# Optimization experiments

Hardware: AMD Instinct MI355X
Metric: run time of the kernel (lower is better)

The kernel has to match this reference:

```python
import jax, jax.numpy as jnp
import numpy as np

B, S, E, H = 2, 2048, 1024, 16
D = E // H  # head_dim = 64


def setup_inputs() -> dict:
    key = jax.random.key(0)
    ks = jax.random.split(key, 5)
    return {
        "hidden_states": jax.random.normal(ks[0], (B, S, E), jnp.float32),
        "c_attn_w": jax.random.normal(ks[1], (E, 3 * E), jnp.float32) * 0.02,
        "c_attn_b": jnp.zeros((3 * E,), jnp.float32),
        "c_proj_w": jax.random.normal(ks[2], (E, E), jnp.float32) * 0.02,
        "c_proj_b": jnp.zeros((E,), jnp.float32),
    }


def reference(hidden_states, c_attn_w, c_attn_b, c_proj_w, c_proj_b):
    # Conv1D: x @ w + b -> qkv [B, S, 3E]
    qkv = hidden_states @ c_attn_w + c_attn_b
    q, k, v = jnp.split(qkv, 3, axis=-1)
    # [B, H, S, D]
    q = q.reshape(B, S, H, D).transpose(0, 2, 1, 3)
    k = k.reshape(B, S, H, D).transpose(0, 2, 1, 3)
    v = v.reshape(B, S, H, D).transpose(0, 2, 1, 3)
    # scores [B, H, S, S], scaled by sqrt(head_dim)
    scores = jnp.einsum("bhqd,bhkd->bhqk", q, k) / jnp.sqrt(jnp.asarray(D, q.dtype))
    causal = jnp.tril(jnp.ones((S, S), bool))  # [S, S]
    mask_value = jnp.finfo(scores.dtype).min
    scores = jnp.where(causal, scores, mask_value)
    attn = jax.nn.softmax(scores, axis=-1)
    # attn @ V -> [B, H, S, D] -> [B, S, E]
    out = jnp.einsum("bhqk,bhkd->bhqd", attn, v)
    out = out.transpose(0, 2, 1, 3).reshape(B, S, E)
    return out @ c_proj_w + c_proj_b
```

## Files before the change

kernel.cpp:

```cpp
#include <hip/hip_runtime.h>

using bf16 = __bf16;
typedef __bf16 bf16x8 __attribute__((ext_vector_type(8)));
typedef __bf16 bf16x4 __attribute__((ext_vector_type(4)));
typedef float  f32x4  __attribute__((ext_vector_type(4)));

#define MFMA16(a, b, c) __builtin_amdgcn_mfma_f32_16x16x32_bf16((a), (b), (c), 0, 0, 0)

static constexpr int S = 2048, E = 1024;
static constexpr float CSCALE = 0.18033688011112042f;

__device__ __forceinline__ void gld16(const bf16* g, bf16* l) {
    __builtin_amdgcn_global_load_lds((const __attribute__((address_space(1))) unsigned*)g,
                                     (__attribute__((address_space(3))) unsigned*)l, 16, 0, 0);
}

__global__ __launch_bounds__(256) void k_prep(const float* __restrict__ hs, const float* __restrict__ w0,
                                              const float* __restrict__ w1, bf16* __restrict__ A0,
                                              bf16* __restrict__ Wt0, bf16* __restrict__ Wt1) {
    __shared__ float tile[32][33];
    const int bx = blockIdx.x;
    if (bx < 4096) {
        int i = (bx * 256 + threadIdx.x) * 4;
        float4 v = *(const float4*)(hs + i);
        bf16x4 o = { (bf16)v.x, (bf16)v.y, (bf16)v.z, (bf16)v.w };
        *(bf16x4*)(A0 + i) = o;
        return;
    }
    const float* in;
    bf16* outp;
    int K, N, nb, kb;
    if (bx < 4096 + 3072) {
        int j = bx - 4096; in = w0; outp = Wt0; K = 1024; N = 3072; nb = j % 96; kb = j / 96;
    } else {
        int j = bx - 7168; in = w1; outp = Wt1; K = 1024; N = 1024; nb = j % 32; kb = j / 32;
    }
    const int bxx = nb * 32, byy = kb * 32;
    const int tx = threadIdx.x & 31, ty = threadIdx.x >> 5;
#pragma unroll
    for (int i = 0; i < 32; i += 8)
        tile[ty + i][tx] = in[(long)(byy + ty + i) * N + bxx + tx];
    __syncthreads();
#pragma unroll
    for (int i = 0; i < 32; i += 8)
        outp[(long)(bxx + ty + i) * K + byy + tx] = (bf16)tile[tx][ty + i];
}

__global__ __launch_bounds__(512, 2) void k_gemm_qkv(const bf16* __restrict__ A, const bf16* __restrict__ Bt,
                                                     const float* __restrict__ bias, bf16* __restrict__ Qs,
                                                     bf16* __restrict__ Kf, bf16* __restrict__ Vf, int Kk) {
    __shared__ __align__(16) char smem[131072];
    bf16* sA = (bf16*)smem;
    bf16* sB = (bf16*)(smem + 65536);

    const int NT = Kk >> 5;

    const int cpx = gridDim.x >> 3;
    const int bid = blockIdx.x;
    const int sid = (bid & 7) * cpx + (bid >> 3);
    const long bm = (long)(sid & 15) * 256;
    const int bnT = sid >> 4;
    const long bn = (long)bnT * 256;

    const int tid = threadIdx.x;
    const int w = tid >> 6, lane = tid & 63;
    const int col = lane & 15, quad = lane >> 4;
    const int wr = w >> 2, wc = w & 3;
    const int wrow = wr * 128, wcol = wc * 64;

    const int c0 = tid, c1 = 512 + tid;
    const int r0 = c0 >> 2, g0 = (c0 & 3) ^ ((r0 >> 1) & 3);
    const int r1 = c1 >> 2, g1 = (c1 & 3) ^ ((r1 >> 1) & 3);
    const bf16* gA0 = A + (bm + r0) * Kk + g0 * 8;
    const bf16* gA1 = A + (bm + r1) * Kk + g1 * 8;
    const bf16* gB0 = Bt + (bn + r0) * Kk + g0 * 8;
    const bf16* gB1 = Bt + (bn + r1) * Kk + g1 * 8;

    f32x4 acc[8][4] = {};

#pragma unroll
    for (int tt = 0; tt < 3; ++tt) {
        bf16* dA = sA + tt * 8192;
        bf16* dB = sB + tt * 8192;
        gld16(gA0 + tt * 32, dA + w * 512);
        gld16(gA1 + tt * 32, dA + 4096 + w * 512);
        gld16(gB0 + tt * 32, dB + w * 512);
        gld16(gB1 + tt * 32, dB + 4096 + w * 512);
    }
    asm volatile("s_waitcnt vmcnt(8)" ::: "memory");
    __builtin_amdgcn_s_barrier();

#pragma unroll 1
    for (int t = 0; t < NT; ++t) {
        const bf16* sAs = sA + (t & 3) * 8192;
        const bf16* sBs = sB + (t & 3) * 8192;
        const int ts = t + 3;
        bf16* dA = sA + (ts & 3) * 8192;
        bf16* dB = sB + (ts & 3) * 8192;

        bf16x8 bfr[4], af[4];
#pragma unroll
        for (int nt = 0; nt < 4; ++nt) {
            const int row = wcol + nt * 16 + col;
            bfr[nt] = *(const bf16x8*)(sBs + row * 32 + ((quad ^ ((row >> 1) & 3)) * 8));
        }
#pragma unroll
        for (int mt = 0; mt < 4; ++mt) {
            const int row = wrow + mt * 16 + col;
            af[mt] = *(const bf16x8*)(sAs + row * 32 + ((quad ^ ((row >> 1) & 3)) * 8));
        }
        if (ts < NT) {
            gld16(gA0 + ts * 32, dA + w * 512);
            gld16(gA1 + ts * 32, dA + 4096 + w * 512);
        }
        __builtin_amdgcn_s_barrier();
        __builtin_amdgcn_s_setprio(1);
#pragma unroll
        for (int mt = 0; mt < 4; ++mt)
#pragma unroll
            for (int nt = 0; nt < 4; ++nt)
                acc[mt][nt] = MFMA16(af[mt], bfr[nt], acc[mt][nt]);
        __builtin_amdgcn_s_setprio(0);
        __builtin_amdgcn_s_barrier();

#pragma unroll
        for (int mt = 0; mt < 4; ++mt) {
            const int row = wrow + 64 + mt * 16 + col;
            af[mt] = *(const bf16x8*)(sAs + row * 32 + ((quad ^ ((row >> 1) & 3)) * 8));
        }
        if (ts < NT) {
            gld16(gB0 + ts * 32, dB + w * 512);
            gld16(gB1 + ts * 32, dB + 4096 + w * 512);
        }
        __builtin_amdgcn_s_barrier();
        __builtin_amdgcn_s_setprio(1);
#pragma unroll
        for (int mt = 0; mt < 4; ++mt)
#pragma unroll
            for (int nt = 0; nt < 4; ++nt)
                acc[4 + mt][nt] = MFMA16(af[mt], bfr[nt], acc[4 + mt][nt]);
        __builtin_amdgcn_s_setprio(0);
        if (t < NT - 3)       asm volatile("s_waitcnt vmcnt(8)" ::: "memory");
        else if (t == NT - 3) asm volatile("s_waitcnt vmcnt(4)" ::: "memory");
        else if (t == NT - 2) asm volatile("s_waitcnt vmcnt(0)" ::: "memory");
        __builtin_amdgcn_s_barrier();
    }

    const int seg = bnT >> 2;

    if (seg == 0) {
#pragma unroll
        for (int nt = 0; nt < 4; ++nt) {
            const long gc = bn + wcol + nt * 16 + col;
            const float bv = bias[gc];
#pragma unroll
            for (int mt = 0; mt < 8; ++mt) {
                const long gr = bm + wrow + mt * 16 + quad * 4;
#pragma unroll
                for (int r = 0; r < 4; ++r)
                    Qs[(gr + r) * 1024 + gc] = (bf16)((acc[mt][nt][r] + bv) * CSCALE);
            }
        }
        return;
    }

    bf16* myT = (bf16*)smem + w * (64 * 72);
    const int bmi = (int)bm;
    const int b = bmi >> 11;
    const int ktw = ((bmi & 2047) >> 6) + wr * 2;
    float bv[4];
#pragma unroll
    for (int nt = 0; nt < 4; ++nt) bv[nt] = bias[bn + wcol + nt * 16 + col];

    if (seg == 1) {
        const int head = (((int)bn - 1024) >> 6) + wc;
        const int bh = b * 16 + head;
#pragma unroll
        for (int p = 0; p < 2; ++p) {
#pragma unroll
            for (int mt2 = 0; mt2 < 4; ++mt2)
#pragma unroll
                for (int nt = 0; nt < 4; ++nt)
#pragma unroll
                    for (int r = 0; r < 4; ++r)
                        myT[(mt2 * 16 + quad * 4 + r) * 72 + nt * 16 + col] =
                            (bf16)(acc[p * 4 + mt2][nt][r] + bv[nt]);
#pragma unroll
            for (int mtp = 0; mtp < 4; ++mtp)
#pragma unroll
                for (int half = 0; half < 2; ++half) {
                    bf16x8 ch = *(const bf16x8*)(myT + (mtp * 16 + col) * 72 + half * 32 + quad * 8);
                    const long chunk = ((long)(bh * 32 + ktw + p) * 8 + mtp * 2 + half) * 64 + lane;
                    *(bf16x8*)(Kf + chunk * 8) = ch;
                }
        }
    } else {
        const int head = (((int)bn - 2048) >> 6) + wc;
        const int bh = b * 16 + head;
#pragma unroll
        for (int p = 0; p < 2; ++p) {
#pragma unroll
            for (int nt = 0; nt < 4; ++nt)
#pragma unroll
                for (int mt2 = 0; mt2 < 4; ++mt2) {
                    bf16x4 pk = { (bf16)(acc[p * 4 + mt2][nt][0] + bv[nt]),
                                  (bf16)(acc[p * 4 + mt2][nt][1] + bv[nt]),
                                  (bf16)(acc[p * 4 + mt2][nt][2] + bv[nt]),
                                  (bf16)(acc[p * 4 + mt2][nt][3] + bv[nt]) };
                    *(bf16x4*)(myT + (nt * 16 + col) * 72 + mt2 * 16 + quad * 4) = pk;
                }
#pragma unroll
            for (int dt = 0; dt < 4; ++dt)
#pragma unroll
                for (int ks = 0; ks < 2; ++ks) {
                    bf16x8 ch = *(const bf16x8*)(myT + (dt * 16 + col) * 72 + ks * 32 + quad * 8);
                    const long chunk = ((long)(bh * 32 + ktw + p) * 8 + dt * 2 + ks) * 64 + lane;
                    *(bf16x8*)(Vf + chunk * 8) = ch;
                }
        }
    }
}

__global__ __launch_bounds__(256) void k_gemm_bt64(const bf16* __restrict__ A, const bf16* __restrict__ Bt,
                                                    const float* __restrict__ bias, float* __restrict__ Cout,
                                                    int Mm, int Nn, int Kk) {
    const int bm = blockIdx.x * 64;
    const int bn = blockIdx.y * 128;
    const int tid = threadIdx.x;
    const int w = tid >> 6, lane = tid & 63;
    const int wm = (w >> 1) * 32, wn = (w & 1) * 64;
    const int col = lane & 15, quad = lane >> 4;

    __shared__ bf16 sA[64 * 64];
    __shared__ bf16 sB[128 * 64];

    const bf16* pA[2]; bf16* lA[2];
#pragma unroll
    for (int i = 0; i < 2; i++) {
        const int c = i * 256 + w * 64 + lane;
        const int r = c >> 3, sl = (c & 7) ^ (r & 7);
        pA[i] = A + (long)(bm + r) * Kk + sl * 8;
        lA[i] = sA + i * 2048 + w * 512;
    }
    const bf16* pB[4]; bf16* lB[4];
#pragma unroll
    for (int i = 0; i < 4; i++) {
        const int c = i * 256 + w * 64 + lane;
        const int r = c >> 3, sl = (c & 7) ^ (r & 7);
        pB[i] = Bt + (long)(bn + r) * Kk + sl * 8;
        lB[i] = sB + i * 2048 + w * 512;
    }

    f32x4 acc[2][4] = {};

    for (int k0 = 0; k0 < Kk; k0 += 64) {
        __syncthreads();
#pragma unroll
        for (int i = 0; i < 2; i++) gld16(pA[i] + k0, lA[i]);
#pragma unroll
        for (int i = 0; i < 4; i++) gld16(pB[i] + k0, lB[i]);
        __syncthreads();
#pragma unroll
        for (int h = 0; h < 2; h++) {
            bf16x8 af[2], bfr[4];
#pragma unroll
            for (int mt = 0; mt < 2; mt++) {
                const int row = wm + mt * 16 + col;
                af[mt] = *(const bf16x8*)(sA + row * 64 + (((h * 4 + quad) ^ (col & 7)) * 8));
            }
#pragma unroll
            for (int nt = 0; nt < 4; nt++) {
                const int row = wn + nt * 16 + col;
                bfr[nt] = *(const bf16x8*)(sB + row * 64 + (((h * 4 + quad) ^ (col & 7)) * 8));
            }
#pragma unroll
            for (int mt = 0; mt < 2; mt++)
#pragma unroll
                for (int nt = 0; nt < 4; nt++)
                    acc[mt][nt] = MFMA16(af[mt], bfr[nt], acc[mt][nt]);
        }
    }

#pragma unroll
    for (int mt = 0; mt < 2; mt++) {
        const int gr = bm + wm + mt * 16 + quad * 4;
#pragma unroll
        for (int nt = 0; nt < 4; nt++) {
            const int gc = bn + wn + nt * 16 + col;
            const float bv = bias[gc];
#pragma unroll
            for (int r = 0; r < 4; r++)
                Cout[(long)(gr + r) * Nn + gc] = acc[mt][nt][r] + bv;
        }
    }
}

__global__ __launch_bounds__(128) void k_attn(const bf16* __restrict__ Qs, const bf16* __restrict__ Kf,
                                              const bf16* __restrict__ Vf, bf16* __restrict__ out) {
    const int bh = blockIdx.x & 31;
    const int tp = blockIdx.x >> 5;
    const int b = bh >> 4, h = bh & 15;
    const int tid = threadIdx.x;
    const int w = tid >> 6, lane = tid & 63;
    const int col = lane & 15, quad = lane >> 4;

    __shared__ bf16 sP[2][32 * 72];
    __shared__ float M[2][64][36];
    bf16* pw = sP[w];

    const bf16* kfb = Kf + ((long)bh << 17) + lane * 8;
    const bf16* vfb = Vf + ((long)bh << 17) + lane * 8;

#pragma unroll 1
    for (int sel = 0; sel < 2; sel++) {
        const int t = sel ? 63 - tp : tp;
        const int q0 = t * 32;
        const int nkt = (t >> 1) + 1;
        const int kA = nkt >> 1;
        const int kbeg = w ? kA : 0;
        const int kend = w ? nkt : kA;

        bf16x8 bq[2][2];
#pragma unroll
        for (int qg = 0; qg < 2; qg++) {
            const bf16* qp = Qs + (long)(b * S + q0 + qg * 16 + col) * E + h * 64 + quad * 8;
            bq[qg][0] = *(const bf16x8*)(qp);
            bq[qg][1] = *(const bf16x8*)(qp + 32);
        }
        float m_[2] = { -1e30f, -1e30f }, l_[2] = { 0.f, 0.f };
        f32x4 o[2][4] = {};

#pragma unroll 1
        for (int kt = kbeg; kt < kend; kt++) {
            bf16x8 kfr[4][2], vfr[4][2];
#pragma unroll
            for (int mt = 0; mt < 4; mt++)
#pragma unroll
                for (int half = 0; half < 2; half++)
                    kfr[mt][half] = *(const bf16x8*)(kfb + ((long)(kt * 8 + mt * 2 + half) << 9));
#pragma unroll
            for (int dt = 0; dt < 4; dt++)
#pragma unroll
                for (int ks = 0; ks < 2; ks++)
                    vfr[dt][ks] = *(const bf16x8*)(vfb + ((long)(kt * 8 + dt * 2 + ks) << 9));

            f32x4 s[2][4];
#pragma unroll
            for (int mt = 0; mt < 4; mt++)
#pragma unroll
                for (int qg = 0; qg < 2; qg++) {
                    f32x4 z = {};
                    z = MFMA16(kfr[mt][0], bq[qg][0], z);
                    z = MFMA16(kfr[mt][1], bq[qg][1], z);
                    s[qg][mt] = z;
                }
            if (kt == nkt - 1) {
#pragma unroll
                for (int qg = 0; qg < 2; qg++) {
                    const int qrow = q0 + qg * 16 + col;
#pragma unroll
                    for (int mt = 0; mt < 4; mt++)
#pragma unroll
                        for (int r = 0; r < 4; r++)
                            if (kt * 64 + mt * 16 + quad * 4 + r > qrow) s[qg][mt][r] = -1e30f;
                }
            }
#pragma unroll
            for (int qg = 0; qg < 2; qg++) {
                float cm = -1e30f;
#pragma unroll
                for (int mt = 0; mt < 4; mt++)
#pragma unroll
                    for (int r = 0; r < 4; r++) cm = fmaxf(cm, s[qg][mt][r]);
                cm = fmaxf(cm, __shfl_xor(cm, 16));
                cm = fmaxf(cm, __shfl_xor(cm, 32));
                const float mnew = fmaxf(m_[qg], cm);
                const float alpha = __builtin_amdgcn_exp2f(m_[qg] - mnew);
                m_[qg] = mnew;
                float rs = 0.f;
#pragma unroll
                for (int mt = 0; mt < 4; mt++)
#pragma unroll
                    for (int r = 0; r < 4; r++) {
                        float pe = __builtin_amdgcn_exp2f(s[qg][mt][r] - mnew);
                        s[qg][mt][r] = pe;
                        rs += pe;
                    }
                l_[qg] = l_[qg] * alpha + rs;
#pragma unroll
                for (int dt = 0; dt < 4; dt++)
#pragma unroll
                    for (int r = 0; r < 4; r++) o[qg][dt][r] *= alpha;
#pragma unroll
                for (int mt = 0; mt < 4; mt++) {
                    bf16x4 pk = { (bf16)s[qg][mt][0], (bf16)s[qg][mt][1],
                                  (bf16)s[qg][mt][2], (bf16)s[qg][mt][3] };
                    *(bf16x4*)(pw + (qg * 16 + col) * 72 + mt * 16 + quad * 4) = pk;
                }
            }
#pragma unroll
            for (int ks = 0; ks < 2; ks++) {
                bf16x8 ap[2];
#pragma unroll
                for (int qg = 0; qg < 2; qg++)
                    ap[qg] = *(const bf16x8*)(pw + (qg * 16 + col) * 72 + ks * 32 + quad * 8);
#pragma unroll
                for (int dt = 0; dt < 4; dt++)
#pragma unroll
                    for (int qg = 0; qg < 2; qg++)
                        o[qg][dt] = MFMA16(vfr[dt][ks], ap[qg], o[qg][dt]);
            }
        }

#pragma unroll
        for (int qg = 0; qg < 2; qg++) {
            float lt = l_[qg];
            lt += __shfl_xor(lt, 16);
            lt += __shfl_xor(lt, 32);
            l_[qg] = lt;
        }

        if (w == 0) {
#pragma unroll
            for (int qg = 0; qg < 2; qg++) {
#pragma unroll
                for (int dt = 0; dt < 4; dt++)
                    *(f32x4*)&M[sel][lane][qg * 16 + dt * 4] = o[qg][dt];
                M[sel][lane][32 + qg * 2] = m_[qg];
                M[sel][lane][33 + qg * 2] = l_[qg];
            }
        }
        __syncthreads();
        if (w == 1) {
#pragma unroll
            for (int qg = 0; qg < 2; qg++) {
                const float m0 = M[sel][lane][32 + qg * 2];
                const float l0 = M[sel][lane][33 + qg * 2];
                const float mm = fmaxf(m0, m_[qg]);
                const float a0 = __builtin_amdgcn_exp2f(m0 - mm);
                const float a1 = __builtin_amdgcn_exp2f(m_[qg] - mm);
                const float li = 1.f / (l0 * a0 + l_[qg] * a1);
                bf16* op = out + (long)(b * S + q0 + qg * 16 + col) * E + h * 64 + quad * 4;
#pragma unroll
                for (int dt = 0; dt < 4; dt++) {
                    f32x4 o0 = *(const f32x4*)&M[sel][lane][qg * 16 + dt * 4];
                    bf16x4 ov;
#pragma unroll
                    for (int r = 0; r < 4; r++)
                        ov[r] = (bf16)((o0[r] * a0 + o[qg][dt][r] * a1) * li);
                    *(bf16x4*)(op + dt * 16) = ov;
                }
            }
        }
    }
}

extern "C" void kernel_launch(void* const* d_in, const int* in_sizes, int n_in,
                              void* d_out, int out_size, void* d_ws, size_t ws_size,
                              hipStream_t stream) {
    const float* hs = (const float*)d_in[0];
    const float* w0 = (const float*)d_in[1];
    const float* b0 = (const float*)d_in[2];
    const float* w1 = (const float*)d_in[3];
    const float* b1 = (const float*)d_in[4];
    float* outp = (float*)d_out;

    char* ws = (char*)d_ws;
    bf16* A0    = (bf16*)(ws);
    bf16* Wt0   = (bf16*)(ws + 8388608);
    bf16* Wt1   = (bf16*)(ws + 14680064);
    bf16* Qs    = (bf16*)(ws + 16777216);
    bf16* Kf    = (bf16*)(ws + 25165824);
    bf16* Vf    = (bf16*)(ws + 33554432);
    bf16* attnO = (bf16*)(ws + 41943040);

    k_prep<<<8192, 256, 0, stream>>>(hs, w0, w1, A0, Wt0, Wt1);
    k_gemm_qkv<<<192, 512, 0, stream>>>(A0, Wt0, b0, Qs, Kf, Vf, 1024);
    k_attn<<<1024, 128, 0, stream>>>(Qs, Kf, Vf, attnO);
    k_gemm_bt64<<<dim3(64, 8), 256, 0, stream>>>(attnO, Wt1, b1, outp, 4096, 1024, 1024);
}
```

Before: 172.8 us.

## Retile QKV GEMM to 128x192 blocks with 6 waves and triple buffering

The QKV projection GEMM moves from 256x256 tiles with 8 waves and a 4-stage buffer to 128x192 tiles with 6 waves and a 3-stage LDS ring. The grid grows from 192 to 512 blocks, which fills the 256 CUs better and lets about 3 blocks sit on each CU thanks to the smaller LDS footprint. Load assignment is redistributed across waves, and the epilogue is simplified to one 64-row pass per wave. The trade-off is less operand reuse per tile and more global and LDS traffic per FLOP.

```diff
diff --git a/kernel.cpp b/kernel.cpp
--- a/kernel.cpp
+++ b/kernel.cpp
@@ -46,73 +46,76 @@
         outp[(long)(bxx + ty + i) * K + byy + tx] = (bf16)tile[tx][ty + i];
 }
 
-__global__ __launch_bounds__(512, 2) void k_gemm_qkv(const bf16* __restrict__ A, const bf16* __restrict__ Bt,
+__global__ __launch_bounds__(384, 3) void k_gemm_qkv(const bf16* __restrict__ A, const bf16* __restrict__ Bt,
                                                      const float* __restrict__ bias, bf16* __restrict__ Qs,
                                                      bf16* __restrict__ Kf, bf16* __restrict__ Vf, int Kk) {
-    __shared__ __align__(16) char smem[131072];
+    __shared__ __align__(16) char smem[61440];
     bf16* sA = (bf16*)smem;
-    bf16* sB = (bf16*)(smem + 65536);
+    bf16* sB = (bf16*)(smem + 24576);
 
     const int NT = Kk >> 5;
 
-    const int cpx = gridDim.x >> 3;
     const int bid = blockIdx.x;
-    const int sid = (bid & 7) * cpx + (bid >> 3);
-    const long bm = (long)(sid & 15) * 256;
-    const int bnT = sid >> 4;
-    const long bn = (long)bnT * 256;
+    const int sid = (bid & 7) * 64 + (bid >> 3);
+    const long bm = (long)(sid & 31) * 128;
+    const long bn = (long)(sid >> 5) * 192;
 
     const int tid = threadIdx.x;
     const int w = tid >> 6, lane = tid & 63;
     const int col = lane & 15, quad = lane >> 4;
-    const int wr = w >> 2, wc = w & 3;
-    const int wrow = wr * 128, wcol = wc * 64;
-
-    const int c0 = tid, c1 = 512 + tid;
-    const int r0 = c0 >> 2, g0 = (c0 & 3) ^ ((r0 >> 1) & 3);
-    const int r1 = c1 >> 2, g1 = (c1 & 3) ^ ((r1 >> 1) & 3);
-    const bf16* gA0 = A + (bm + r0) * Kk + g0 * 8;
-    const bf16* gA1 = A + (bm + r1) * Kk + g1 * 8;
-    const bf16* gB0 = Bt + (bn + r0) * Kk + g0 * 8;
-    const bf16* gB1 = Bt + (bn + r1) * Kk + g1 * 8;
-
-    f32x4 acc[8][4] = {};
-
-#pragma unroll
-    for (int tt = 0; tt < 3; ++tt) {
-        bf16* dA = sA + tt * 8192;
-        bf16* dB = sB + tt * 8192;
-        gld16(gA0 + tt * 32, dA + w * 512);
-        gld16(gA1 + tt * 32, dA + 4096 + w * 512);
-        gld16(gB0 + tt * 32, dB + w * 512);
-        gld16(gB1 + tt * 32, dB + 4096 + w * 512);
-    }
-    asm volatile("s_waitcnt vmcnt(8)" ::: "memory");
+    const int wc = w % 3, wr = w / 3;
+    const int wrow = wr * 64, wcol = wc * 64;
+
+    const int nch = (w < 2) ? 4 : 3;
+    const bf16* gsrc[4];
+    bf16* ldst[4];
+    int sstep[4];
+#pragma unroll
+    for (int j = 0; j < 4; ++j) {
+        const int c = w + 6 * j;
+        const bool a = (c < 8);
+        const int cl = a ? c : (c - 8);
+        const int r = cl * 16 + (lane >> 2);
+        const int kc = (lane & 3) ^ ((r >> 1) & 3);
+        gsrc[j] = (a ? A + (bm + r) * Kk : Bt + (bn + r) * Kk) + kc * 8;
+        ldst[j] = (a ? sA : sB) + r * 32 + (lane & 3) * 8;
+        sstep[j] = a ? 4096 : 6144;
+    }
+
+    f32x4 acc[4][4] = {};
+
+#pragma unroll
+    for (int tt = 0; tt < 2; ++tt)
+#pragma unroll
+        for (int j = 0; j < 4; ++j)
+            if (j < nch) gld16(gsrc[j] + tt * 32, ldst[j] + tt * sstep[j]);
+    if (w < 2) asm volatile("s_waitcnt vmcnt(4)" ::: "memory");
+    else       asm volatile("s_waitcnt vmcnt(3)" ::: "memory");
     __builtin_amdgcn_s_barrier();
 
+    int slot = 0, wslot = 2;
 #pragma unroll 1
     for (int t = 0; t < NT; ++t) {
-        const bf16* sAs = sA + (t & 3) * 8192;
-        const bf16* sBs = sB + (t & 3) * 8192;
-        const int ts = t + 3;
-        bf16* dA = sA + (ts & 3) * 8192;
-        bf16* dB = sB + (ts & 3) * 8192;
-
-        bf16x8 bfr[4], af[4];
+        const bf16* sAs = sA + slot * 4096;
+        const bf16* sBs = sB + slot * 6144;
+
+        if (t + 2 < NT) {
+#pragma unroll
+            for (int j = 0; j < 4; ++j)
+                if (j < nch) gld16(gsrc[j] + (t + 2) * 32, ldst[j] + wslot * sstep[j]);
+        }
+
+        bf16x8 af[4], bfr[4];
+#pragma unroll
+        for (int mt = 0; mt < 4; ++mt) {
+            const int row = wrow + mt * 16 + col;
+            af[mt] = *(const bf16x8*)(sAs + row * 32 + ((quad ^ ((row >> 1) & 3)) * 8));
+        }
 #pragma unroll
         for (int nt = 0; nt < 4; ++nt) {
             const int row = wcol + nt * 16 + col;
             bfr[nt] = *(const bf16x8*)(sBs + row * 32 + ((quad ^ ((row >> 1) & 3)) * 8));
         }
-#pragma unroll
-        for (int mt = 0; mt < 4; ++mt) {
-            const int row = wrow + mt * 16 + col;
-            af[mt] = *(const bf16x8*)(sAs + row * 32 + ((quad ^ ((row >> 1) & 3)) * 8));
-        }
-        if (ts < NT) {
-            gld16(gA0 + ts * 32, dA + w * 512);
-            gld16(gA1 + ts * 32, dA + 4096 + w * 512);
-        }
         __builtin_amdgcn_s_barrier();
         __builtin_amdgcn_s_setprio(1);
 #pragma unroll
@@ -121,103 +124,79 @@
             for (int nt = 0; nt < 4; ++nt)
                 acc[mt][nt] = MFMA16(af[mt], bfr[nt], acc[mt][nt]);
         __builtin_amdgcn_s_setprio(0);
+        if (t < NT - 2) {
+            if (w < 2) asm volatile("s_waitcnt vmcnt(4)" ::: "memory");
+            else       asm volatile("s_waitcnt vmcnt(3)" ::: "memory");
+        } else {
+            asm volatile("s_waitcnt vmcnt(0)" ::: "memory");
+        }
         __builtin_amdgcn_s_barrier();
 
-#pragma unroll
-        for (int mt = 0; mt < 4; ++mt) {
-            const int row = wrow + 64 + mt * 16 + col;
-            af[mt] = *(const bf16x8*)(sAs + row * 32 + ((quad ^ ((row >> 1) & 3)) * 8));
-        }
-        if (ts < NT) {
-            gld16(gB0 + ts * 32, dB + w * 512);
-            gld16(gB1 + ts * 32, dB + 4096 + w * 512);
-        }
-        __builtin_amdgcn_s_barrier();
-        __builtin_amdgcn_s_setprio(1);
-#pragma unroll
-        for (int mt = 0; mt < 4; ++mt)
-#pragma unroll
-            for (int nt = 0; nt < 4; ++nt)
-                acc[4 + mt][nt] = MFMA16(af[mt], bfr[nt], acc[4 + mt][nt]);
-        __builtin_amdgcn_s_setprio(0);
-        if (t < NT - 3)       asm volatile("s_waitcnt vmcnt(8)" ::: "memory");
-        else if (t == NT - 3) asm volatile("s_waitcnt vmcnt(4)" ::: "memory");
-        else if (t == NT - 2) asm volatile("s_waitcnt vmcnt(0)" ::: "memory");
-        __builtin_amdgcn_s_barrier();
-    }
-
-    const int seg = bnT >> 2;
+        slot = (slot == 2) ? 0 : slot + 1;
+        wslot = (wslot == 2) ? 0 : wslot + 1;
+    }
+
+    const long gc0 = bn + wcol;
+    const int seg = (int)(gc0 >> 10);
+    float bv[4];
+#pragma unroll
+    for (int nt = 0; nt < 4; ++nt) bv[nt] = bias[gc0 + nt * 16 + col];
 
     if (seg == 0) {
 #pragma unroll
         for (int nt = 0; nt < 4; ++nt) {
-            const long gc = bn + wcol + nt * 16 + col;
-            const float bv = bias[gc];
-#pragma unroll
-            for (int mt = 0; mt < 8; ++mt) {
+            const long gc = gc0 + nt * 16 + col;
+#pragma unroll
+            for (int mt = 0; mt < 4; ++mt) {
                 const long gr = bm + wrow + mt * 16 + quad * 4;
 #pragma unroll
                 for (int r = 0; r < 4; ++r)
-                    Qs[(gr + r) * 1024 + gc] = (bf16)((acc[mt][nt][r] + bv) * CSCALE);
+                    Qs[(gr + r) * 1024 + gc] = (bf16)((acc[mt][nt][r] + bv[nt]) * CSCALE);
             }
         }
         return;
     }
 
-    bf16* myT = (bf16*)smem + w * (64 * 72);
+    bf16* myT = (bf16*)smem + w * 4608;
     const int bmi = (int)bm;
     const int b = bmi >> 11;
-    const int ktw = ((bmi & 2047) >> 6) + wr * 2;
-    float bv[4];
-#pragma unroll
-    for (int nt = 0; nt < 4; ++nt) bv[nt] = bias[bn + wcol + nt * 16 + col];
+    const int ktw = ((bmi & 2047) >> 6) + wr;
+    const int head = (int)((gc0 & 1023) >> 6);
+    const int bh = b * 16 + head;
 
     if (seg == 1) {
-        const int head = (((int)bn - 1024) >> 6) + wc;
-        const int bh = b * 16 + head;
-#pragma unroll
-        for (int p = 0; p < 2; ++p) {
-#pragma unroll
-            for (int mt2 = 0; mt2 < 4; ++mt2)
-#pragma unroll
-                for (int nt = 0; nt < 4; ++nt)
-#pragma unroll
-                    for (int r = 0; r < 4; ++r)
-                        myT[(mt2 * 16 + quad * 4 + r) * 72 + nt * 16 + col] =
-                            (bf16)(acc[p * 4 + mt2][nt][r] + bv[nt]);
-#pragma unroll
-            for (int mtp = 0; mtp < 4; ++mtp)
-#pragma unroll
-                for (int half = 0; half < 2; ++half) {
-                    bf16x8 ch = *(const bf16x8*)(myT + (mtp * 16 + col) * 72 + half * 32 + quad * 8);
-                    const long chunk = ((long)(bh * 32 + ktw + p) * 8 + mtp * 2 + half) * 64 + lane;
-                    *(bf16x8*)(Kf + chunk * 8) = ch;
-                }
-        }
+#pragma unroll
+        for (int mt = 0; mt < 4; ++mt)
+#pragma unroll
+            for (int nt = 0; nt < 4; ++nt)
+#pragma unroll
+                for (int r = 0; r < 4; ++r)
+                    myT[(mt * 16 + quad * 4 + r) * 72 + nt * 16 + col] = (bf16)(acc[mt][nt][r] + bv[nt]);
+#pragma unroll
+        for (int mtp = 0; mtp < 4; ++mtp)
+#pragma unroll
+            for (int half = 0; half < 2; ++half) {
+                bf16x8 ch = *(const bf16x8*)(myT + (mtp * 16 + col) * 72 + half * 32 + quad * 8);
+                const long chunk = ((long)(bh * 32 + ktw) * 8 + mtp * 2 + half) * 64 + lane;
+                *(bf16x8*)(Kf + chunk * 8) = ch;
+            }
     } else {
-        const int head = (((int)bn - 2048) >> 6) + wc;
-        const int bh = b * 16 + head;
-#pragma unroll
-        for (int p = 0; p < 2; ++p) {
-#pragma unroll
-            for (int nt = 0; nt < 4; ++nt)
-#pragma unroll
-                for (int mt2 = 0; mt2 < 4; ++mt2) {
-                    bf16x4 pk = { (bf16)(acc[p * 4 + mt2][nt][0] + bv[nt]),
-                                  (bf16)(acc[p * 4 + mt2][nt][1] + bv[nt]),
-                                  (bf16)(acc[p * 4 + mt2][nt][2] + bv[nt]),
-                                  (bf16)(acc[p * 4 + mt2][nt][3] + bv[nt]) };
-                    *(bf16x4*)(myT + (nt * 16 + col) * 72 + mt2 * 16 + quad * 4) = pk;
-                }
-#pragma unroll
-            for (int dt = 0; dt < 4; ++dt)
-#pragma unroll
-                for (int ks = 0; ks < 2; ++ks) {
-                    bf16x8 ch = *(const bf16x8*)(myT + (dt * 16 + col) * 72 + ks * 32 + quad * 8);
-                    const long chunk = ((long)(bh * 32 + ktw + p) * 8 + dt * 2 + ks) * 64 + lane;
-                    *(bf16x8*)(Vf + chunk * 8) = ch;
-                }
-        }
+#pragma unroll
+        for (int nt = 0; nt < 4; ++nt)
+#pragma unroll
+            for (int mt = 0; mt < 4; ++mt) {
+                bf16x4 pk = { (bf16)(acc[mt][nt][0] + bv[nt]), (bf16)(acc[mt][nt][1] + bv[nt]),
+                              (bf16)(acc[mt][nt][2] + bv[nt]), (bf16)(acc[mt][nt][3] + bv[nt]) };
+                *(bf16x4*)(myT + (nt * 16 + col) * 72 + mt * 16 + quad * 4) = pk;
+            }
+#pragma unroll
+        for (int dt = 0; dt < 4; ++dt)
+#pragma unroll
+            for (int ks = 0; ks < 2; ++ks) {
+                bf16x8 ch = *(const bf16x8*)(myT + (dt * 16 + col) * 72 + ks * 32 + quad * 8);
+                const long chunk = ((long)(bh * 32 + ktw) * 8 + dt * 2 + ks) * 64 + lane;
+                *(bf16x8*)(Vf + chunk * 8) = ch;
+            }
     }
 }
 
@@ -475,7 +454,7 @@
     bf16* attnO = (bf16*)(ws + 41943040);
 
     k_prep<<<8192, 256, 0, stream>>>(hs, w0, w1, A0, Wt0, Wt1);
-    k_gemm_qkv<<<192, 512, 0, stream>>>(A0, Wt0, b0, Qs, Kf, Vf, 1024);
+    k_gemm_qkv<<<512, 384, 0, stream>>>(A0, Wt0, b0, Qs, Kf, Vf, 1024);
     k_attn<<<1024, 128, 0, stream>>>(Qs, Kf, Vf, attnO);
     k_gemm_bt64<<<dim3(64, 8), 256, 0, stream>>>(attnO, Wt1, b1, outp, 4096, 1024, 1024);
 }
```

Result: slower. 179.0 us (+3.6%).
